# Optimization experiments

Measured on AMD Instinct MI355X. Metric: run time of the kernel, lower is better.

Reference implementation:

```python
import jax, jax.numpy as jnp
import numpy as np

N_NODES = 100000
N_EDGES = 1600000
IN_FEATS = 512
OUT_FEATS = 128


def setup_inputs() -> dict:
    key = jax.random.key(0)
    k1, k2, k3, k4, k5 = jax.random.split(key, 5)
    feat = jax.random.normal(k1, (N_NODES, IN_FEATS), dtype=jnp.float32)
    src = jax.random.randint(k2, (N_EDGES,), 0, N_NODES, dtype=jnp.int32)
    dst = jax.random.randint(k3, (N_EDGES,), 0, N_NODES, dtype=jnp.int32)
    edge_weight = jax.random.uniform(k4, (N_EDGES,), dtype=jnp.float32)
    # xavier_uniform init for the [in, out] weight
    limit = float(np.sqrt(6.0 / (IN_FEATS + OUT_FEATS)))
    weight = jax.random.uniform(k5, (IN_FEATS, OUT_FEATS), dtype=jnp.float32,
                                minval=-limit, maxval=limit)
    bias = jnp.zeros((OUT_FEATS,), dtype=jnp.float32)
    return {"feat": feat, "weight": weight, "bias": bias,
            "edge_weight": edge_weight, "src": src, "dst": dst}


def reference(feat, weight, bias, edge_weight, src, dst):
    n = feat.shape[0]
    ones = jnp.ones_like(edge_weight)
    # degrees from edge list; clamp(min=1)
    out_deg = jnp.maximum(jax.ops.segment_sum(ones, src, num_segments=n), 1.0)
    in_deg = jnp.maximum(jax.ops.segment_sum(ones, dst, num_segments=n), 1.0)
    # norm='both': left-normalize source feats by out_deg^-0.5
    feat_src = feat * jax.lax.rsqrt(out_deg)[:, None]
    # in_feats > out_feats -> project before aggregation
    h = feat_src @ weight                      # [N, OUT]
    msg = h[src] * edge_weight[:, None]        # u_mul_e, [E, OUT]
    rst = jax.ops.segment_sum(msg, dst, num_segments=n)  # fn.sum per dst
    # right-normalize by in_deg^-0.5, add bias (activation is None)
    rst = rst * jax.lax.rsqrt(in_deg)[:, None] + bias
    return rst
```

## Files before the change

### kernel.cpp

```cpp
#include <hip/hip_runtime.h>
#include <hip/hip_bf16.h>

#define NNODES 100000
#define NEDGES 1600000
#define INF 512
#define OUTF 128
#define NB 391
#define BCAP 5120
#define SEG 4096
#define BK 32
#define NKSTEP (INF / BK)

typedef __attribute__((ext_vector_type(8))) __bf16 bf16x8;
typedef __attribute__((ext_vector_type(4))) float f32x4;
typedef __attribute__((ext_vector_type(2))) float f32x2;

typedef const __attribute__((address_space(1))) unsigned int* gas_ptr;
typedef __attribute__((address_space(3))) unsigned int* las_ptr;

__device__ __forceinline__ void gload_lds16(const void* g, void* l) {
  __builtin_amdgcn_global_load_lds((gas_ptr)g, (las_ptr)l, 16, 0, 0);
}

__global__ void wt_kernel(const float* __restrict__ w, unsigned short* __restrict__ wta) {
  int i = blockIdx.x * blockDim.x + threadIdx.x;
  if (i >= 8192) return;
  int lg  = i & 3;
  int l15 = (i >> 2) & 15;
  int c   = (i >> 6) & 7;
  int kb  = i >> 9;
  int n = c * 16 + l15;
  int kbase = kb * 32 + lg * 8;
  unsigned short tmp[8];
#pragma unroll
  for (int j = 0; j < 8; ++j) {
    __bf16 b = (__bf16)(w[(size_t)(kbase + j) * OUTF + n]);
    tmp[j] = __builtin_bit_cast(unsigned short, b);
  }
  ((int4*)wta)[i] = *(int4*)tmp;
}

__global__ __launch_bounds__(256) void bucket_kernel(
    const int* __restrict__ src, const int* __restrict__ dst,
    const float* __restrict__ ew, int* __restrict__ out_cnt,
    int* __restrict__ bucket_cnt, int2* __restrict__ bucket) {
  __shared__ int hist[NB];
  __shared__ int base[NB];
  int t = threadIdx.x;
  for (int i = t; i < NB; i += 256) hist[i] = 0;
  __syncthreads();
  int e0 = blockIdx.x * SEG;
  int e1 = min(e0 + SEG, NEDGES);
  for (int e = e0 + t; e < e1; e += 256) {
    atomicAdd(&out_cnt[src[e]], 1);
    atomicAdd(&hist[dst[e] >> 8], 1);
  }
  __syncthreads();
  for (int i = t; i < NB; i += 256) {
    int c = hist[i];
    base[i] = c ? atomicAdd(&bucket_cnt[i], c) : 0;
    hist[i] = 0;
  }
  __syncthreads();
  for (int e = e0 + t; e < e1; e += 256) {
    int d = dst[e];
    int b = d >> 8;
    int r = atomicAdd(&hist[b], 1);
    int2 en;
    en.x = ((d & 255) << 17) | src[e];
    en.y = __float_as_int(ew[e]);
    bucket[(size_t)b * BCAP + base[b] + r] = en;
  }
}

__global__ __launch_bounds__(512) void bscan_kernel(const int* __restrict__ bucket_cnt,
                                                    int* __restrict__ bucket_base,
                                                    int* __restrict__ rowptr) {
  __shared__ int s[512];
  int t = threadIdx.x;
  int v = (t < NB) ? bucket_cnt[t] : 0;
  s[t] = v;
  __syncthreads();
  for (int off = 1; off < 512; off <<= 1) {
    int x = (t >= off) ? s[t - off] : 0;
    __syncthreads();
    s[t] += x;
    __syncthreads();
  }
  if (t < NB) bucket_base[t] = s[t] - v;
  if (t == 0) rowptr[NNODES] = NEDGES;
}

__global__ __launch_bounds__(256) void csr_kernel(
    const int* __restrict__ bucket_cnt, const int* __restrict__ bucket_base,
    const int2* __restrict__ bucket, int* __restrict__ rowptr,
    int2* __restrict__ epair) {
  __shared__ int hist[256];
  __shared__ int cur[256];
  int b = blockIdx.x;
  int t = threadIdx.x;
  int nb = bucket_cnt[b];
  int bbase = bucket_base[b];
  const int2* bk = bucket + (size_t)b * BCAP;
  hist[t] = 0;
  __syncthreads();
  for (int i = t; i < nb; i += 256) atomicAdd(&hist[bk[i].x >> 17], 1);
  __syncthreads();
  int v = hist[t];
  for (int off = 1; off < 256; off <<= 1) {
    int x = (t >= off) ? hist[t - off] : 0;
    __syncthreads();
    hist[t] += x;
    __syncthreads();
  }
  int excl = hist[t] - v;
  int node = b * 256 + t;
  if (node < NNODES) rowptr[node] = bbase + excl;
  cur[t] = excl;
  __syncthreads();
  for (int i = t; i < nb; i += 256) {
    int2 en = bk[i];
    int nl = en.x >> 17;
    int r = atomicAdd(&cur[nl], 1);
    epair[bbase + r] = make_int2(en.x & 0x1FFFF, en.y);
  }
}

__global__ __launch_bounds__(256, 3) void gemm_kernel(
    const float* __restrict__ feat, const unsigned short* __restrict__ wta,
    const int* __restrict__ out_cnt, unsigned short* __restrict__ h) {
  __shared__ float As[2][128 * BK];
  __shared__ unsigned short Bs[2][4096];

  const int t = threadIdx.x;
  const int lane = t & 63;
  const int wave = t >> 6;
  const int l15 = lane & 15;
  const int lg  = lane >> 4;
  const int rowbase = blockIdx.x * 128;

  const int srow_off = lane >> 3;
  const int schunk = (lane & 7) ^ srow_off;

  int r0 = rowbase + wave * 32 + l15;
  int r1 = r0 + 16;
  float s0 = rsqrtf(fmaxf((float)out_cnt[min(r0, NNODES - 1)], 1.0f));
  float s1 = rsqrtf(fmaxf((float)out_cnt[min(r1, NNODES - 1)], 1.0f));

  f32x4 acc[2][8];
#pragma unroll
  for (int f = 0; f < 2; ++f)
#pragma unroll
    for (int c = 0; c < 8; ++c) acc[f][c] = (f32x4){0.f, 0.f, 0.f, 0.f};

#define STAGE(buf, kb)                                                         \
  {                                                                            \
    _Pragma("unroll")                                                          \
    for (int q = 0; q < 4; ++q) {                                              \
      int gr = min(rowbase + wave * 32 + q * 8 + srow_off, NNODES - 1);        \
      const float* gsrc = feat + (size_t)gr * INF + (kb) * BK + schunk * 4;    \
      gload_lds16(gsrc, &As[buf][(wave * 4 + q) * 256]);                       \
    }                                                                          \
    _Pragma("unroll")                                                          \
    for (int q = 0; q < 2; ++q) {                                              \
      const unsigned short* gsrc =                                             \
          wta + (size_t)(kb) * 4096 + (wave * 2 + q) * 512 + lane * 8;         \
      gload_lds16(gsrc, &Bs[buf][(wave * 2 + q) * 512]);                       \
    }                                                                          \
  }

  int buf = 0;
  STAGE(0, 0);
  __syncthreads();

  for (int kb = 0; kb < NKSTEP; ++kb) {
    if (kb + 1 < NKSTEP) STAGE(buf ^ 1, kb + 1);

    bf16x8 bfr[8];
#pragma unroll
    for (int c = 0; c < 8; ++c)
      bfr[c] = *(const bf16x8*)&Bs[buf][c * 512 + l15 * 32 + lg * 8];

    bf16x8 afr[2];
#pragma unroll
    for (int rf = 0; rf < 2; ++rf) {
      int r = wave * 32 + rf * 16 + l15;
      int c0 = (lg * 2) ^ (l15 & 7);
      int c1 = (lg * 2 + 1) ^ (l15 & 7);
      f32x4 u = *(const f32x4*)&As[buf][r * 32 + c0 * 4];
      f32x4 v = *(const f32x4*)&As[buf][r * 32 + c1 * 4];
      float s = rf ? s1 : s0;
      bf16x8 a;
#pragma unroll
      for (int j = 0; j < 4; ++j) {
        a[j]     = (__bf16)(u[j] * s);
        a[j + 4] = (__bf16)(v[j] * s);
      }
      afr[rf] = a;
    }

#pragma unroll
    for (int c = 0; c < 8; ++c) {
      acc[0][c] = __builtin_amdgcn_mfma_f32_16x16x32_bf16(afr[0], bfr[c], acc[0][c], 0, 0, 0);
      acc[1][c] = __builtin_amdgcn_mfma_f32_16x16x32_bf16(afr[1], bfr[c], acc[1][c], 0, 0, 0);
    }

    __syncthreads();
    buf ^= 1;
  }
#undef STAGE

#pragma unroll
  for (int f = 0; f < 2; ++f) {
    int rb = rowbase + wave * 32 + f * 16 + lg * 4;
#pragma unroll
    for (int r = 0; r < 4; ++r) {
      int row = rb + r;
      if (row < NNODES) {
#pragma unroll
        for (int c = 0; c < 8; ++c) {
          __bf16 bv = (__bf16)acc[f][c][r];
          h[(size_t)row * OUTF + c * 16 + l15] = __builtin_bit_cast(unsigned short, bv);
        }
      }
    }
  }
}

__global__ __launch_bounds__(256) void gather_kernel(
    const int* __restrict__ rowptr, const int2* __restrict__ epair,
    const unsigned short* __restrict__ h, const float* __restrict__ bias,
    float* __restrict__ out) {
  int node = (blockIdx.x * blockDim.x + threadIdx.x) >> 6;
  int lane = threadIdx.x & 63;
  if (node >= NNODES) return;
  int beg = rowptr[node];
  int end = rowptr[node + 1];

  float ax = 0.f, ay = 0.f;
  for (int base = beg; base < end; base += 64) {
    int j = base + lane;
    int2 pr = make_int2(0, 0);
    if (j < end) pr = epair[j];
    int cnt = min(end - base, 64);
    int t = 0;
    for (; t + 4 <= cnt; t += 4) {
      int s0 = __shfl(pr.x, t);
      int s1 = __shfl(pr.x, t + 1);
      int s2 = __shfl(pr.x, t + 2);
      int s3 = __shfl(pr.x, t + 3);
      float w0 = __int_as_float(__shfl(pr.y, t));
      float w1 = __int_as_float(__shfl(pr.y, t + 1));
      float w2 = __int_as_float(__shfl(pr.y, t + 2));
      float w3 = __int_as_float(__shfl(pr.y, t + 3));
      unsigned int u0 = *((const unsigned int*)(h + (size_t)s0 * OUTF) + lane);
      unsigned int u1 = *((const unsigned int*)(h + (size_t)s1 * OUTF) + lane);
      unsigned int u2 = *((const unsigned int*)(h + (size_t)s2 * OUTF) + lane);
      unsigned int u3 = *((const unsigned int*)(h + (size_t)s3 * OUTF) + lane);
      ax += __uint_as_float(u0 << 16) * w0 + __uint_as_float(u1 << 16) * w1 +
            __uint_as_float(u2 << 16) * w2 + __uint_as_float(u3 << 16) * w3;
      ay += __uint_as_float(u0 & 0xFFFF0000u) * w0 + __uint_as_float(u1 & 0xFFFF0000u) * w1 +
            __uint_as_float(u2 & 0xFFFF0000u) * w2 + __uint_as_float(u3 & 0xFFFF0000u) * w3;
    }
    for (; t < cnt; ++t) {
      int s = __shfl(pr.x, t);
      float w = __int_as_float(__shfl(pr.y, t));
      unsigned int u = *((const unsigned int*)(h + (size_t)s * OUTF) + lane);
      ax += __uint_as_float(u << 16) * w;
      ay += __uint_as_float(u & 0xFFFF0000u) * w;
    }
  }

  float sc = rsqrtf(fmaxf((float)(end - beg), 1.0f));
  f32x2 b = *((const f32x2*)bias + lane);
  f32x2 r;
  r.x = ax * sc + b.x;
  r.y = ay * sc + b.y;
  *((f32x2*)(out + (size_t)node * OUTF) + lane) = r;
}

extern "C" void kernel_launch(void* const* d_in, const int* in_sizes, int n_in,
                              void* d_out, int out_size, void* d_ws, size_t ws_size,
                              hipStream_t stream) {
  const float* feat   = (const float*)d_in[0];
  const float* weight = (const float*)d_in[1];
  const float* bias   = (const float*)d_in[2];
  const float* ew     = (const float*)d_in[3];
  const int*   src    = (const int*)d_in[4];
  const int*   dst    = (const int*)d_in[5];
  float* out = (float*)d_out;
  char* ws = (char*)d_ws;

  int* out_cnt        = (int*)ws;
  int* rowptr         = (int*)(ws + 0x80000);
  int* bucket_cnt     = (int*)(ws + 0x100000);
  int* bucket_base    = (int*)(ws + 0x101000);
  unsigned short* wta = (unsigned short*)(ws + 0x110000);
  int2* bucket        = (int2*)(ws + 0x140000);
  int2* epair         = (int2*)(ws + 0x1200000);
  unsigned short* h   = (unsigned short*)(ws + 0x2000000);

  hipMemsetAsync(out_cnt, 0, NNODES * sizeof(int), stream);
  hipMemsetAsync(bucket_cnt, 0, NB * sizeof(int), stream);

  wt_kernel<<<32, 256, 0, stream>>>(weight, wta);
  bucket_kernel<<<(NEDGES + SEG - 1) / SEG, 256, 0, stream>>>(src, dst, ew, out_cnt,
                                                              bucket_cnt, bucket);
  bscan_kernel<<<1, 512, 0, stream>>>(bucket_cnt, bucket_base, rowptr);
  csr_kernel<<<NB, 256, 0, stream>>>(bucket_cnt, bucket_base, bucket, rowptr, epair);
  gemm_kernel<<<(NNODES + 127) / 128, 256, 0, stream>>>(feat, wta, out_cnt, h);
  gather_kernel<<<(NNODES * 64 + 255) / 256, 256, 0, stream>>>(rowptr, epair, h, bias, out);
}
```

Measured before the change: 256.9 us.

## Read GEMM B operand directly from global; restructure gather into 4-edge-parallel wave

```diff
diff --git a/kernel.cpp b/kernel.cpp
--- a/kernel.cpp
+++ b/kernel.cpp
@@ -130,7 +130,6 @@
     const float* __restrict__ feat, const unsigned short* __restrict__ wta,
     const int* __restrict__ out_cnt, unsigned short* __restrict__ h) {
   __shared__ float As[2][128 * BK];
-  __shared__ unsigned short Bs[2][4096];
 
   const int t = threadIdx.x;
   const int lane = t & 63;
@@ -153,7 +152,7 @@
 #pragma unroll
     for (int c = 0; c < 8; ++c) acc[f][c] = (f32x4){0.f, 0.f, 0.f, 0.f};
 
-#define STAGE(buf, kb)                                                         \
+#define STAGE_A(buf, kb)                                                       \
   {                                                                            \
     _Pragma("unroll")                                                          \
     for (int q = 0; q < 4; ++q) {                                              \
@@ -161,25 +160,19 @@
       const float* gsrc = feat + (size_t)gr * INF + (kb) * BK + schunk * 4;    \
       gload_lds16(gsrc, &As[buf][(wave * 4 + q) * 256]);                       \
     }                                                                          \
-    _Pragma("unroll")                                                          \
-    for (int q = 0; q < 2; ++q) {                                              \
-      const unsigned short* gsrc =                                             \
-          wta + (size_t)(kb) * 4096 + (wave * 2 + q) * 512 + lane * 8;         \
-      gload_lds16(gsrc, &Bs[buf][(wave * 2 + q) * 512]);                       \
-    }                                                                          \
   }
 
   int buf = 0;
-  STAGE(0, 0);
+  STAGE_A(0, 0);
   __syncthreads();
 
   for (int kb = 0; kb < NKSTEP; ++kb) {
-    if (kb + 1 < NKSTEP) STAGE(buf ^ 1, kb + 1);
+    if (kb + 1 < NKSTEP) STAGE_A(buf ^ 1, kb + 1);
 
     bf16x8 bfr[8];
 #pragma unroll
     for (int c = 0; c < 8; ++c)
-      bfr[c] = *(const bf16x8*)&Bs[buf][c * 512 + l15 * 32 + lg * 8];
+      bfr[c] = *(const bf16x8*)(wta + (size_t)kb * 4096 + c * 512 + l15 * 32 + lg * 8);
 
     bf16x8 afr[2];
 #pragma unroll
@@ -208,7 +201,7 @@
     __syncthreads();
     buf ^= 1;
   }
-#undef STAGE
+#undef STAGE_A
 
 #pragma unroll
   for (int f = 0; f < 2; ++f) {
@@ -227,56 +220,75 @@
   }
 }
 
+__device__ __forceinline__ float blo(unsigned int u) { return __uint_as_float(u << 16); }
+__device__ __forceinline__ float bhi(unsigned int u) { return __uint_as_float(u & 0xFFFF0000u); }
+
 __global__ __launch_bounds__(256) void gather_kernel(
     const int* __restrict__ rowptr, const int2* __restrict__ epair,
     const unsigned short* __restrict__ h, const float* __restrict__ bias,
     float* __restrict__ out) {
-  int node = (blockIdx.x * blockDim.x + threadIdx.x) >> 6;
-  int lane = threadIdx.x & 63;
-  if (node >= NNODES) return;
-  int beg = rowptr[node];
-  int end = rowptr[node + 1];
-
-  float ax = 0.f, ay = 0.f;
-  for (int base = beg; base < end; base += 64) {
-    int j = base + lane;
-    int2 pr = make_int2(0, 0);
-    if (j < end) pr = epair[j];
-    int cnt = min(end - base, 64);
-    int t = 0;
-    for (; t + 4 <= cnt; t += 4) {
-      int s0 = __shfl(pr.x, t);
-      int s1 = __shfl(pr.x, t + 1);
-      int s2 = __shfl(pr.x, t + 2);
-      int s3 = __shfl(pr.x, t + 3);
-      float w0 = __int_as_float(__shfl(pr.y, t));
-      float w1 = __int_as_float(__shfl(pr.y, t + 1));
-      float w2 = __int_as_float(__shfl(pr.y, t + 2));
-      float w3 = __int_as_float(__shfl(pr.y, t + 3));
-      unsigned int u0 = *((const unsigned int*)(h + (size_t)s0 * OUTF) + lane);
-      unsigned int u1 = *((const unsigned int*)(h + (size_t)s1 * OUTF) + lane);
-      unsigned int u2 = *((const unsigned int*)(h + (size_t)s2 * OUTF) + lane);
-      unsigned int u3 = *((const unsigned int*)(h + (size_t)s3 * OUTF) + lane);
-      ax += __uint_as_float(u0 << 16) * w0 + __uint_as_float(u1 << 16) * w1 +
-            __uint_as_float(u2 << 16) * w2 + __uint_as_float(u3 << 16) * w3;
-      ay += __uint_as_float(u0 & 0xFFFF0000u) * w0 + __uint_as_float(u1 & 0xFFFF0000u) * w1 +
-            __uint_as_float(u2 & 0xFFFF0000u) * w2 + __uint_as_float(u3 & 0xFFFF0000u) * w3;
-    }
-    for (; t < cnt; ++t) {
-      int s = __shfl(pr.x, t);
-      float w = __int_as_float(__shfl(pr.y, t));
-      unsigned int u = *((const unsigned int*)(h + (size_t)s * OUTF) + lane);
-      ax += __uint_as_float(u << 16) * w;
-      ay += __uint_as_float(u & 0xFFFF0000u) * w;
-    }
-  }
-
-  float sc = rsqrtf(fmaxf((float)(end - beg), 1.0f));
-  f32x2 b = *((const f32x2*)bias + lane);
-  f32x2 r;
-  r.x = ax * sc + b.x;
-  r.y = ay * sc + b.y;
-  *((f32x2*)(out + (size_t)node * OUTF) + lane) = r;
+  const int lane = threadIdx.x & 63;
+  const int grp  = lane >> 4;
+  const int li   = lane & 15;
+  const int wid  = (blockIdx.x * blockDim.x + threadIdx.x) >> 6;
+  const int nw   = (gridDim.x * blockDim.x) >> 6;
+
+  for (int node = wid; node < NNODES; node += nw) {
+    const int beg = rowptr[node];
+    const int end = rowptr[node + 1];
+
+    float a0 = 0.f, a1 = 0.f, a2 = 0.f, a3 = 0.f;
+    float a4 = 0.f, a5 = 0.f, a6 = 0.f, a7 = 0.f;
+
+    int e = beg + grp;
+#define GSTEP(pr)                                                              \
+      {                                                                        \
+        const unsigned int* hp =                                               \
+            (const unsigned int*)(h + (size_t)(pr).x * OUTF) + li * 4;         \
+        uint4 u = *(const uint4*)hp;                                           \
+        float w = __int_as_float((pr).y);                                      \
+        a0 += blo(u.x) * w; a1 += bhi(u.x) * w;                                \
+        a2 += blo(u.y) * w; a3 += bhi(u.y) * w;                                \
+        a4 += blo(u.z) * w; a5 += bhi(u.z) * w;                                \
+        a6 += blo(u.w) * w; a7 += bhi(u.w) * w;                                \
+      }
+    for (; e + 12 < end; e += 16) {
+      int2 p0 = epair[e];
+      int2 p1 = epair[e + 4];
+      int2 p2 = epair[e + 8];
+      int2 p3 = epair[e + 12];
+      GSTEP(p0); GSTEP(p1); GSTEP(p2); GSTEP(p3);
+    }
+    for (; e < end; e += 4) {
+      int2 p = epair[e];
+      GSTEP(p);
+    }
+#undef GSTEP
+
+    a0 += __shfl_xor(a0, 16); a1 += __shfl_xor(a1, 16);
+    a2 += __shfl_xor(a2, 16); a3 += __shfl_xor(a3, 16);
+    a4 += __shfl_xor(a4, 16); a5 += __shfl_xor(a5, 16);
+    a6 += __shfl_xor(a6, 16); a7 += __shfl_xor(a7, 16);
+    a0 += __shfl_xor(a0, 32); a1 += __shfl_xor(a1, 32);
+    a2 += __shfl_xor(a2, 32); a3 += __shfl_xor(a3, 32);
+    a4 += __shfl_xor(a4, 32); a5 += __shfl_xor(a5, 32);
+    a6 += __shfl_xor(a6, 32); a7 += __shfl_xor(a7, 32);
+
+    float sc = rsqrtf(fmaxf((float)(end - beg), 1.0f));
+    if (grp == 0) {
+      f32x4 bv = ((const f32x4*)bias)[li * 2];
+      f32x4 r;
+      r.x = a0 * sc + bv.x; r.y = a1 * sc + bv.y;
+      r.z = a2 * sc + bv.z; r.w = a3 * sc + bv.w;
+      ((f32x4*)(out + (size_t)node * OUTF))[li * 2] = r;
+    } else if (grp == 1) {
+      f32x4 bv = ((const f32x4*)bias)[li * 2 + 1];
+      f32x4 r;
+      r.x = a4 * sc + bv.x; r.y = a5 * sc + bv.y;
+      r.z = a6 * sc + bv.z; r.w = a7 * sc + bv.w;
+      ((f32x4*)(out + (size_t)node * OUTF))[li * 2 + 1] = r;
+    }
+  }
 }
 
 extern "C" void kernel_launch(void* const* d_in, const int* in_sizes, int n_in,
@@ -309,5 +321,5 @@
   bscan_kernel<<<1, 512, 0, stream>>>(bucket_cnt, bucket_base, rowptr);
   csr_kernel<<<NB, 256, 0, stream>>>(bucket_cnt, bucket_base, bucket, rowptr, epair);
   gemm_kernel<<<(NNODES + 127) / 128, 256, 0, stream>>>(feat, wta, out_cnt, h);
-  gather_kernel<<<(NNODES * 64 + 255) / 256, 256, 0, stream>>>(rowptr, epair, h, bias, out);
-}
+  gather_kernel<<<1024, 256, 0, stream>>>(rowptr, epair, h, bias, out);
+}
```

Result: slower. 270.1 us (+5.1%).
